# Kernel optimization log

Measured on AMD Instinct MI355X. Metric: run time of the kernel, lower is better.

The kernel has to match this reference:

```python
import jax, jax.numpy as jnp
import numpy as np

S, B, E, H, Q, T, K, N = 256, 32, 768, 1024, 64, 512, 11, 16
STD = 2.5
EPS = 1e-5


def gaussian_kernel(size, std):
    t = np.linspace(-(size - 1) / 2, (size - 1) / 2, size)
    x, y = np.meshgrid(t, t)
    kern = np.exp(-0.5 * (x ** 2 + y ** 2) / std ** 2)
    return (kern / kern.sum()).astype(np.float32)


def setup_inputs() -> dict:
    key = jax.random.key(0)
    ks = jax.random.split(key, 24)
    s = 0.05
    inp = {
        'sentence_batch': jax.random.normal(ks[0], (S, B, E), jnp.float32),
        # forward LSTM params (torch layout: W_ih (4H,E), W_hh (4H,H), gate order i,f,g,o)
        'Wih_f': jax.random.normal(ks[1], (4 * H, E), jnp.float32) * s,
        'Whh_f': jax.random.normal(ks[2], (4 * H, H), jnp.float32) * s,
        'bih_f': jnp.zeros((4 * H,), jnp.float32),
        'bhh_f': jnp.zeros((4 * H,), jnp.float32),
        # backward LSTM params
        'Wih_b': jax.random.normal(ks[3], (4 * H, E), jnp.float32) * s,
        'Whh_b': jax.random.normal(ks[4], (4 * H, H), jnp.float32) * s,
        'bih_b': jnp.zeros((4 * H,), jnp.float32),
        'bhh_b': jnp.zeros((4 * H,), jnp.float32),
        # layer norms
        'g_in': jnp.ones((E,), jnp.float32), 'be_in': jnp.zeros((E,), jnp.float32),
        'g_fw': jnp.ones((H,), jnp.float32), 'be_fw': jnp.zeros((H,), jnp.float32),
        'g_bk': jnp.ones((H,), jnp.float32), 'be_bk': jnp.zeros((H,), jnp.float32),
        'g_sq': jnp.ones((2 * Q,), jnp.float32), 'be_sq': jnp.zeros((2 * Q,), jnp.float32),
        # squeeze + topic linears (torch layout: W (out,in))
        'Wsq': jax.random.normal(ks[5], (Q, H), jnp.float32) * s,
        'bsq': jnp.zeros((Q,), jnp.float32),
        'Wtop': jax.random.normal(ks[6], (T, 2 * Q), jnp.float32) * s,
        'btop': jnp.zeros((T,), jnp.float32),
        'gauss_kern': jnp.asarray(gaussian_kernel(K, STD)),
    }
    return inp


def layer_norm(x, g, b):
    mu = jnp.mean(x, axis=-1, keepdims=True)
    var = jnp.mean((x - mu) ** 2, axis=-1, keepdims=True)
    return g * (x - mu) * jax.lax.rsqrt(var + EPS) + b


def lstm(x, Wih, Whh, bih, bhh):
    # x: (S, B, E) -> hidden states (S, B, H). torch gate order: i, f, g, o.
    h0 = jnp.zeros((x.shape[1], Whh.shape[1]), x.dtype)
    c0 = jnp.zeros_like(h0)
    xg = jnp.einsum('sbe,ge->sbg', x, Wih) + bih  # precompute input gates

    def step(carry, xt):
        h, c = carry
        gates = xt + h @ Whh.T + bhh
        i, f, g, o = jnp.split(gates, 4, axis=-1)
        c = jax.nn.sigmoid(f) * c + jax.nn.sigmoid(i) * jnp.tanh(g)
        h = jax.nn.sigmoid(o) * jnp.tanh(c)
        return (h, c), h

    _, hs = jax.lax.scan(step, (h0, c0), xg)
    return hs


def batch_pca(e, dim):
    # e: (S, B, F) -> projections (B, S, dim) onto top-dim principal axes
    c = e - jnp.mean(e, axis=0)
    cov = jnp.einsum('sbi,sbj->bij', c, c) / e.shape[0]  # (B, F, F), symmetric
    _, evecs = jnp.linalg.eigh(cov)  # ascending eigenvalues
    top = evecs[:, :, ::-1][:, :, :dim]  # (B, F, dim), descending order
    return jnp.einsum('sbf,bfn->bsn', c, top)


def gauss_smooth(x, kern):
    # x: (B, S, N) smoothed with 2D gaussian, SAME padding
    p = (kern.shape[0] - 1) // 2
    y = jax.lax.conv_general_dilated(
        x[:, None, :, :], kern[None, None, :, :], (1, 1), [(p, p), (p, p)])
    return y[:, 0]


def adj_cos(e):
    # cosine similarity between adjacent sequence positions: (B, S, N) -> (B, S-1)
    a, b = e[:, :-1], e[:, 1:]
    num = jnp.sum(a * b, axis=-1)
    den = jnp.linalg.norm(a, axis=-1) * jnp.linalg.norm(b, axis=-1)
    return num / den


def reference(sentence_batch, Wih_f, Whh_f, bih_f, bhh_f, Wih_b, Whh_b, bih_b, bhh_b,
              g_in, be_in, g_fw, be_fw, g_bk, be_bk, g_sq, be_sq,
              Wsq, bsq, Wtop, btop, gauss_kern):
    x = layer_norm(sentence_batch, g_in, be_in)
    x_f = lstm(x, Wih_f, Whh_f, bih_f, bhh_f)
    x_b = lstm(x[::-1], Wih_b, Whh_b, bih_b, bhh_b)[::-1]
    x_f = layer_norm(x_f, g_fw, be_fw)
    x_b = layer_norm(x_b, g_bk, be_bk)
    x_f = jnp.tanh(jnp.einsum('sbh,qh->sbq', x_f, Wsq) + bsq)
    x_b = jnp.tanh(jnp.einsum('sbh,qh->sbq', x_b, Wsq) + bsq)
    xc = layer_norm(jnp.concatenate((x_f, x_b), axis=-1), g_sq, be_sq)
    topic_preds = jnp.einsum('sbq,tq->sbt', xc, Wtop) + btop

    # segmentation path (no-grad in original)
    e_f = batch_pca(jax.lax.stop_gradient(x_f), N)
    e_b = batch_pca(jax.lax.stop_gradient(x_b), N)
    e_f = gauss_smooth(e_f, gauss_kern)
    e_b = gauss_smooth(e_b, gauss_kern)
    d = jnp.sqrt(adj_cos(e_f) * adj_cos(e_b))  # (B, S-1)
    pos = jnp.argmax(d, axis=1)
    return topic_preds, pos
```

## Files before the change

kernel.cpp:

```cpp
#include <hip/hip_runtime.h>
#include <cstdint>
#include <cstddef>

#define SS   256
#define BB   32
#define EE   768
#define HH   1024
#define QQ   64
#define TTOP 512
#define NPC  16
#define G4   4096
#define TCHUNK 32
#define NBLK 256
#define EPSF 1e-5f

#define OFF_XNT   ((size_t)0)
#define OFF_WHHT  ((size_t)6291456)
#define OFF_CT    ((size_t)14680064)
#define OFF_HBUF  ((size_t)14745600)
#define OFF_CNT   ((size_t)14876672)
#define OFF_XG    ((size_t)14877184)
#define OFF_HS    ((size_t)23265792)
#define OFF_XQ    ((size_t)40043008)
#define OFF_CMAT  ((size_t)0)
#define OFF_COV   ((size_t)1048576)
#define OFF_PG    ((size_t)1310720)
#define OFF_COS   ((size_t)1376256)

#define WLKS 4616
#define LSTM_DYN_LDS 161536

#define AST 65
#define EIG_DYN_LDS 133120

#define EPS32D    5.9604644775390625e-8
#define EPS232D   (EPS32D*EPS32D)
#define SAFMIN32D 1.1754943508222875e-38

__device__ __forceinline__ float sigm(float x){ return 1.0f/(1.0f + expf(-x)); }

__device__ __forceinline__ double wsumd(double v){
  #pragma unroll
  for (int o = 32; o; o >>= 1) v += __shfl_xor(v, o, 64);
  return v;
}
__device__ __forceinline__ double wmaxd(double v){
  #pragma unroll
  for (int o = 32; o; o >>= 1) v = fmax(v, __shfl_xor(v, o, 64));
  return v;
}
__device__ __forceinline__ void dlartg_(double f, double g, double& c, double& s, double& r){
  if (g == 0.0){ c = 1.0; s = 0.0; r = f; }
  else if (f == 0.0){ c = 0.0; s = (g >= 0.0) ? 1.0 : -1.0; r = fabs(g); }
  else {
    double d = sqrt(f*f + g*g);
    c = fabs(f)/d;
    r = copysign(d, f);
    s = g/r;
  }
}
__device__ void dlaev2_(double a, double b, double c,
                        double& rt1, double& rt2, double& cs1, double& sn1){
  double sm = a + c, df = a - c, adf = fabs(df), tb = b + b, ab = fabs(tb);
  double acmx, acmn;
  if (fabs(a) > fabs(c)){ acmx = a; acmn = c; } else { acmx = c; acmn = a; }
  double rt;
  if (adf > ab)      rt = adf*sqrt(1.0 + (ab/adf)*(ab/adf));
  else if (adf < ab) rt = ab*sqrt(1.0 + (adf/ab)*(adf/ab));
  else               rt = ab*sqrt(2.0);
  int sgn1;
  if (sm < 0.0){ rt1 = 0.5*(sm - rt); sgn1 = -1; rt2 = (acmx/rt1)*acmn - (b/rt1)*b; }
  else if (sm > 0.0){ rt1 = 0.5*(sm + rt); sgn1 = 1; rt2 = (acmx/rt1)*acmn - (b/rt1)*b; }
  else { rt1 = 0.5*rt; rt2 = -0.5*rt; sgn1 = 1; }
  double cs; int sgn2;
  if (df >= 0.0){ cs = df + rt; sgn2 = 1; } else { cs = df - rt; sgn2 = -1; }
  double acs = fabs(cs);
  if (acs > ab){ double ct = -tb/cs; sn1 = 1.0/sqrt(1.0+ct*ct); cs1 = ct*sn1; }
  else {
    if (ab == 0.0){ cs1 = 1.0; sn1 = 0.0; }
    else { double tn = -cs/tb; cs1 = 1.0/sqrt(1.0+tn*tn); sn1 = tn*cs1; }
  }
  if (sgn1 == sgn2){ double tn = cs1; cs1 = -sn1; sn1 = tn; }
}

__device__ void dsteqr16_(int base, double* d, double* e, double* z16, int ln){
  if (ln < 16){
    #pragma unroll
    for (int j = 0; j < 16; j++) z16[ln*17+j] = (ln==j) ? 1.0 : 0.0;
  }
  const int n = 16, nm1 = 15;
  int jtot = 0; const int nmaxit = 480;
  int l1 = 0;
  while (l1 < n){
    if (l1 > 0) e[base+l1-1] = 0.0;
    int m = nm1;
    for (int mm = l1; mm < nm1; mm++){
      double tst = fabs(e[base+mm]);
      if (tst == 0.0){ m = mm; break; }
      if (tst <= (sqrt(fabs(d[base+mm]))*sqrt(fabs(d[base+mm+1])))*EPS32D){
        e[base+mm] = 0.0; m = mm; break;
      }
    }
    int l = l1, lend = m;
    l1 = m + 1;
    if (lend == l) continue;
    if (fabs(d[base+lend]) < fabs(d[base+l])){ int t = l; l = lend; lend = t; }
    if (lend > l){
      for (;;){
        int mm = lend;
        for (int k2 = l; k2 < lend; k2++){
          double tst = e[base+k2]*e[base+k2];
          if (tst <= (EPS232D*fabs(d[base+k2]))*fabs(d[base+k2+1]) + SAFMIN32D){ mm = k2; break; }
        }
        if (mm < lend) e[base+mm] = 0.0;
        double p = d[base+l];
        if (mm == l){ l++; if (l <= lend) continue; break; }
        if (mm == l+1){
          double rt1, rt2, cc, ss;
          dlaev2_(d[base+l], e[base+l], d[base+l+1], rt1, rt2, cc, ss);
          if (ln < 16){
            double x = z16[ln*17+l], y = z16[ln*17+l+1];
            z16[ln*17+l]   = cc*x + ss*y;
            z16[ln*17+l+1] = cc*y - ss*x;
          }
          d[base+l] = rt1; d[base+l+1] = rt2; e[base+l] = 0.0;
          l += 2; if (l <= lend) continue; break;
        }
        if (jtot == nmaxit) break;
        jtot++;
        double g = (d[base+l+1]-p)/(2.0*e[base+l]);
        double r = sqrt(g*g+1.0);
        g = d[base+mm] - p + e[base+l]/(g + copysign(r, g));
        double s2 = 1.0, c2 = 1.0; p = 0.0;
        for (int i = mm-1; i >= l; i--){
          double f = s2*e[base+i], b = c2*e[base+i];
          dlartg_(g, f, c2, s2, r);
          if (i != mm-1) e[base+i+1] = r;
          g = d[base+i+1] - p;
          r = (d[base+i]-g)*s2 + 2.0*c2*b;
          p = s2*r;
          d[base+i+1] = g + p;
          g = c2*r - b;
          if (ln < 16){
            double x = z16[ln*17+i], y = z16[ln*17+i+1];
            z16[ln*17+i]   = c2*x - s2*y;
            z16[ln*17+i+1] = s2*x + c2*y;
          }
        }
        d[base+l] -= p; e[base+l] = g;
      }
    } else {
      for (;;){
        int mm = lend;
        for (int k2 = l; k2 > lend; k2--){
          double tst = e[base+k2-1]*e[base+k2-1];
          if (tst <= (EPS232D*fabs(d[base+k2]))*fabs(d[base+k2-1]) + SAFMIN32D){ mm = k2; break; }
        }
        if (mm > lend) e[base+mm-1] = 0.0;
        double p = d[base+l];
        if (mm == l){ l--; if (l >= lend) continue; break; }
        if (mm == l-1){
          double rt1, rt2, cc, ss;
          dlaev2_(d[base+l-1], e[base+l-1], d[base+l], rt1, rt2, cc, ss);
          if (ln < 16){
            double x = z16[ln*17+l-1], y = z16[ln*17+l];
            z16[ln*17+l-1] = cc*x + ss*y;
            z16[ln*17+l]   = cc*y - ss*x;
          }
          d[base+l-1] = rt1; d[base+l] = rt2; e[base+l-1] = 0.0;
          l -= 2; if (l >= lend) continue; break;
        }
        if (jtot == nmaxit) break;
        jtot++;
        double g = (d[base+l-1]-p)/(2.0*e[base+l-1]);
        double r = sqrt(g*g+1.0);
        g = d[base+mm] - p + e[base+l-1]/(g + copysign(r, g));
        double s2 = 1.0, c2 = 1.0; p = 0.0;
        for (int i = mm; i <= l-1; i++){
          double f = s2*e[base+i], b = c2*e[base+i];
          dlartg_(g, f, c2, s2, r);
          if (i != mm) e[base+i-1] = r;
          g = d[base+i] - p;
          r = (d[base+i+1]-g)*s2 + 2.0*c2*b;
          p = s2*r;
          d[base+i] = g + p;
          g = c2*r - b;
          if (ln < 16){
            double x = z16[ln*17+i], y = z16[ln*17+i+1];
            z16[ln*17+i]   = c2*x + s2*y;
            z16[ln*17+i+1] = c2*y - s2*x;
          }
        }
        d[base+l] -= p; e[base+l-1] = g;
      }
    }
  }
  for (int ii = 1; ii < n; ii++){
    int i = ii-1, k = i; double p = d[base+i];
    for (int j = ii; j < n; j++) if (d[base+j] < p){ k = j; p = d[base+j]; }
    if (k != i){
      d[base+k] = d[base+i]; d[base+i] = p;
      if (ln < 16){ double t = z16[ln*17+i]; z16[ln*17+i] = z16[ln*17+k]; z16[ln*17+k] = t; }
    }
  }
}

__device__ void dc_merge(int base, int n1, int n2, double rho_in, int tid,
    double* s_d, double* Zt, double* Tt,
    double* md, double* mz, double* dl, double* wz, double* lam, double* zh,
    double* ev, double* su4, int* indx, int* sec, int* defl, int* prm,
    int* sKn){
  const int ln = tid & 63, w = tid >> 6;
  int n = n1 + n2;
  double zv = 0.0;
  if (ln < n){
    if (ln < n1) zv = Zt[(size_t)(base+n1-1)*AST + base + ln];
    else         zv = Zt[(size_t)(base+n1)*AST + base + ln];
    if (rho_in < 0.0 && ln >= n1) zv = -zv;
  }
  zv *= 0.70710678118654752440;
  mz[ln] = (ln < n) ? zv : 0.0;
  md[ln] = (ln < n) ? s_d[base+ln] : 0.0;
  __syncthreads();
  double rho = fabs(2.0*rho_in);
  if (tid == 0){
    int i1 = 0, i2 = n1, k = 0;
    while (i1 < n1 && i2 < n){
      if (md[i2] < md[i1]) indx[k++] = i2++; else indx[k++] = i1++;
    }
    while (i1 < n1) indx[k++] = i1++;
    while (i2 < n)  indx[k++] = i2++;
  }
  __syncthreads();
  double dmax = wmaxd((ln<n) ? fabs(md[ln]) : 0.0);
  double zmax = wmaxd((ln<n) ? fabs(mz[ln]) : 0.0);
  double tol = 8.0*EPS32D*fmax(dmax, zmax);
  if (w == 0){
    int K = 0, ndefl = 0, pj = -1;
    for (int j = 0; j < n; j++){
      int nj = indx[j];
      if (rho*fabs(mz[nj]) <= tol){
        defl[ndefl++] = nj;
      } else if (pj < 0){
        pj = nj;
      } else {
        double sG = mz[pj], cG = mz[nj];
        double tau = sqrt(cG*cG + sG*sG);
        double tdf = md[nj] - md[pj];
        double c = cG/tau, s = -sG/tau;
        if (fabs(tdf*c*s) <= tol){
          mz[nj] = tau; mz[pj] = 0.0;
          if (ln < n){
            double x = Zt[(size_t)(base+ln)*AST + base+pj];
            double y = Zt[(size_t)(base+ln)*AST + base+nj];
            Zt[(size_t)(base+ln)*AST + base+pj] = c*x + s*y;
            Zt[(size_t)(base+ln)*AST + base+nj] = c*y - s*x;
          }
          double t2 = md[pj]*c*c + md[nj]*s*s;
          double t3 = md[pj]*s*s + md[nj]*c*c;
          md[nj] = t3; md[pj] = t2;
          defl[ndefl++] = pj;
          pj = nj;
        } else {
          sec[K] = pj; dl[K] = md[pj]; wz[K] = mz[pj]; K++;
          pj = nj;
        }
      }
    }
    if (pj >= 0){ sec[K] = pj; dl[K] = md[pj]; wz[K] = mz[pj]; K++; }
    if (ln == 0){ sKn[0] = K; sKn[1] = ndefl; }
  }
  __syncthreads();
  const int K = sKn[0], ndefl = sKn[1];
  double wsum2 = wsumd((ln < K) ? wz[ln]*wz[ln] : 0.0);
  if (ln < K){
    double lo = dl[ln];
    double hi = (ln < K-1) ? dl[ln+1] : (dl[K-1] + rho*wsum2);
    for (int it = 0; it < 120; it++){
      double mid = 0.5*(lo+hi);
      if (!(mid > lo) || !(mid < hi)) break;
      double fv = 1.0;
      for (int i2 = 0; i2 < K; i2++) fv += rho*wz[i2]*wz[i2]/(dl[i2]-mid);
      if (fv < 0.0) lo = mid; else hi = mid;
    }
    double lj = 0.5*(lo+hi);
    if (!(lj > dl[ln])) lj = nextafter(dl[ln], 1.0e300);
    lam[ln] = lj;
  }
  __syncthreads();
  if (ln < K){
    double di = dl[ln];
    double prod = lam[K-1] - di;
    for (int j2 = 0; j2 < ln; j2++)   prod *= (lam[j2]-di)/(dl[j2]-di);
    for (int j2 = ln; j2 < K-1; j2++) prod *= (lam[j2]-di)/(dl[j2+1]-di);
    zh[ln] = copysign(sqrt(fabs(prod)), wz[ln]);
  }
  __syncthreads();
  for (int j = w; j < K; j += 4){
    double ui = (ln < K) ? zh[ln]/(dl[ln]-lam[j]) : 0.0;
    double nrm = sqrt(wsumd(ui*ui));
    su4[w*64 + ln] = ui/nrm;
    if (ln < n){
      double acc = 0.0;
      for (int i2 = 0; i2 < K; i2++)
        acc += Zt[(size_t)(base+ln)*AST + base + sec[i2]]*su4[w*64 + i2];
      Tt[(size_t)ln*AST + j] = acc;
    }
    if (ln == 0) ev[j] = lam[j];
  }
  __syncthreads();
  for (int j = 0; j < ndefl; j++){
    int cj = defl[j];
    if (ln < n) Tt[(size_t)ln*AST + K + j] = Zt[(size_t)(base+ln)*AST + base + cj];
    if (ln == 0) ev[K+j] = md[cj];
  }
  __syncthreads();
  if (tid == 0){
    for (int i2 = 0; i2 < n; i2++) prm[i2] = i2;
    for (int a2 = 0; a2 < n-1; a2++){
      int kk = a2;
      for (int b2 = a2+1; b2 < n; b2++) if (ev[prm[b2]] < ev[prm[kk]]) kk = b2;
      int t3 = prm[a2]; prm[a2] = prm[kk]; prm[kk] = t3;
    }
  }
  __syncthreads();
  if (ln < n){
    for (int c2 = 0; c2 < n; c2++)
      Zt[(size_t)(base+ln)*AST + base + c2] = Tt[(size_t)ln*AST + prm[c2]];
  }
  if (ln == 0){ for (int c2 = 0; c2 < n; c2++) s_d[base+c2] = ev[prm[c2]]; }
  __syncthreads();
}

__global__ __launch_bounds__(256) void k_eig(const float* __restrict__ covg,
                                             float* __restrict__ Pg){
  int u = blockIdx.x, tid = threadIdx.x;
  const int ln = tid & 63, w = tid >> 6;
  extern __shared__ double dsm[];
  double* A  = dsm;
  double* Qh = dsm + 4160;
  double* Zt = dsm + 8320;
  double* Tt = dsm + 12480;
  __shared__ double s_d[64], s_e[64], s_tau[64], s_v[64], s_w[64];
  __shared__ double md[64], mz[64], dl[64], wz[64], lam[64], zh[64], ev[64];
  __shared__ double su4[4*64];
  __shared__ double z16a[4*272];
  __shared__ int indx[64], sec[64], defl[64], prm[64], sKn[2];

  for (int n = tid; n < 4096; n += 256)
    A[(n >> 6)*AST + (n & 63)] = (double)covg[(size_t)u*4096 + n];
  __syncthreads();

  for (int i = 0; i < 63; i++){
    double alpha = A[(size_t)(i+1)*AST + i];
    double xv = (ln >= i+2) ? A[(size_t)ln*AST + i] : 0.0;
    double xnorm2 = wsumd(xv*xv);
    if (xnorm2 == 0.0){
      if (tid == 0){ s_e[i] = alpha; s_tau[i] = 0.0; }
    } else {
      double beta = -copysign(sqrt(alpha*alpha + xnorm2), alpha);
      double taui = (beta - alpha)/beta;
      double sc = 1.0/(alpha - beta);
      s_v[ln] = (ln == i+1) ? 1.0 : ((ln >= i+2) ? A[(size_t)ln*AST+i]*sc : 0.0);
      __syncthreads();
      if (ln >= i+2) A[(size_t)ln*AST+i] = s_v[ln];
      double wr = 0.0;
      if (ln >= i+1){
        for (int c2 = i+1; c2 < 64; c2++){
          double av = (ln >= c2) ? A[(size_t)ln*AST+c2] : A[(size_t)c2*AST+ln];
          wr += av*s_v[c2];
        }
        wr *= taui;
      }
      double dotwv = wsumd((ln >= i+1) ? wr*s_v[ln] : 0.0);
      double alp2 = -0.5*taui*dotwv;
      wr += alp2*s_v[ln];
      s_w[ln] = (ln >= i+1) ? wr : 0.0;
      __syncthreads();
      if (ln >= i+1){
        for (int c2 = i+1; c2 <= ln; c2++)
          if ((c2 & 3) == w)
            A[(size_t)ln*AST+c2] -= s_v[ln]*s_w[c2] + s_w[ln]*s_v[c2];
      }
      if (tid == 0){ s_e[i] = beta; s_tau[i] = taui; }
    }
    __syncthreads();
  }
  if (w == 0) s_d[ln] = A[(size_t)ln*AST+ln];
  __syncthreads();

  for (int n = tid; n < 4160; n += 256) Qh[n] = 0.0;
  __syncthreads();
  if (w == 0) Qh[(size_t)ln*AST+ln] = 1.0;
  __syncthreads();
  for (int i = 62; i >= 0; i--){
    double taui = s_tau[i];
    if (taui != 0.0){
      s_v[ln] = (ln == i+1) ? 1.0 : ((ln >= i+2) ? A[(size_t)ln*AST+i] : 0.0);
      __syncthreads();
      double dj = 0.0;
      for (int r2 = i+1; r2 < 64; r2++) dj += s_v[r2]*Qh[(size_t)r2*AST+ln];
      dj *= taui;
      for (int r2 = i+1; r2 < 64; r2++)
        if ((r2 & 3) == w)
          Qh[(size_t)r2*AST+ln] -= s_v[r2]*dj;
    }
    __syncthreads();
  }

  double rho_a = s_e[15], rho_b = s_e[47], rho_top = s_e[31];
  if (tid == 0){
    s_d[15] -= fabs(rho_a);   s_d[16] -= fabs(rho_a);
    s_d[31] -= fabs(rho_top); s_d[32] -= fabs(rho_top);
    s_d[47] -= fabs(rho_b);   s_d[48] -= fabs(rho_b);
  }
  for (int n = tid; n < 4160; n += 256) Zt[n] = 0.0;
  __syncthreads();
  dsteqr16_(w*16, s_d, s_e, &z16a[w*272], ln);
  if (ln < 16){
    for (int j = 0; j < 16; j++)
      Zt[(size_t)(w*16+ln)*AST + w*16 + j] = z16a[w*272 + ln*17+j];
  }
  __syncthreads();

  dc_merge(0, 16, 16, rho_a, tid, s_d, Zt, Tt, md, mz, dl, wz, lam, zh, ev, su4, indx, sec, defl, prm, sKn);
  dc_merge(32, 16, 16, rho_b, tid, s_d, Zt, Tt, md, mz, dl, wz, lam, zh, ev, su4, indx, sec, defl, prm, sKn);
  dc_merge(0, 32, 32, rho_top, tid, s_d, Zt, Tt, md, mz, dl, wz, lam, zh, ev, su4, indx, sec, defl, prm, sKn);

  for (int nn = w; nn < 16; nn += 4){
    double acc = 0.0;
    for (int k = 0; k < 64; k++)
      acc += Qh[(size_t)ln*AST+k]*Zt[(size_t)k*AST + (63-nn)];
    Pg[(size_t)u*1024 + ln*16 + nn] = (float)acc;
  }
}

__global__ void k_ln_in(const float* __restrict__ x, const float* __restrict__ g,
                        const float* __restrict__ be, float* __restrict__ xnT){
  int bid = blockIdx.x; int s = bid >> 5, b = bid & 31;
  int tid = threadIdx.x;
  const float* row = x + ((size_t)(s*BB + b))*EE;
  __shared__ float r1[256], r2[256];
  float su = 0.f, sq = 0.f;
  for (int e = tid; e < EE; e += 256){ float v = row[e]; su += v; sq += v*v; }
  r1[tid] = su; r2[tid] = sq; __syncthreads();
  for (int st = 128; st > 0; st >>= 1){
    if (tid < st){ r1[tid] += r1[tid+st]; r2[tid] += r2[tid+st]; }
    __syncthreads();
  }
  float mu  = r1[0] * (1.0f/EE);
  float var = r2[0] * (1.0f/EE) - mu*mu;
  float rstd = rsqrtf(var + EPSF);
  for (int e = tid; e < EE; e += 256){
    float v = (row[e]-mu)*rstd*g[e] + be[e];
    xnT[((size_t)s*EE + e)*BB + b] = v;
  }
}

__global__ void k_whht(const float* __restrict__ Whh_f, const float* __restrict__ Whh_b,
                       float* __restrict__ WhhT){
  int d  = blockIdx.z;
  const float* Whh = d ? Whh_b : Whh_f;
  int rt = blockIdx.x*32, kt = blockIdx.y*32;
  int tx = threadIdx.x & 31, ty = threadIdx.x >> 5;
  __shared__ float tile[32][33];
  for (int i = ty; i < 32; i += 8)
    tile[i][tx] = Whh[(size_t)(rt+i)*HH + kt+tx];
  __syncthreads();
  for (int i = ty; i < 32; i += 8)
    WhhT[((size_t)d*HH + kt+i)*G4 + rt+tx] = tile[tx][i];
}

__global__ void k_zero(float* __restrict__ p, int n){
  int i = blockIdx.x*blockDim.x + threadIdx.x;
  if (i < n) p[i] = 0.f;
}

__global__ __launch_bounds__(256) void k_xg(const float* __restrict__ xnT,
        const float* __restrict__ Wih_f, const float* __restrict__ Wih_b,
        float* __restrict__ xg, int* __restrict__ cnt, int c){
  if (blockIdx.x == 0 && blockIdx.y == 0 && threadIdx.x < 17)
    __hip_atomic_store(&cnt[threadIdx.x*16], 0, __ATOMIC_RELAXED, __HIP_MEMORY_SCOPE_AGENT);
  int nb = blockIdx.x, rb = blockIdx.y;
  int d = rb >> 5, rloc0 = (rb & 31)*128;
  const float* Wih = d ? Wih_b : Wih_f;
  int tid = threadIdx.x;
  int tx = tid & 15, ty = tid >> 4;
  __shared__ float Al[16*132];
  __shared__ float Bl[16*132];
  float acc[8][8];
  #pragma unroll
  for (int i = 0; i < 8; i++)
    #pragma unroll
    for (int j = 0; j < 8; j++) acc[i][j] = 0.f;
  for (int kc = 0; kc < EE; kc += 16){
    #pragma unroll
    for (int j = 0; j < 8; j++){
      int idx = tid + j*256;
      int n = idx & 127, k = idx >> 7;
      int tglob = c*TCHUNK + nb*4 + (n >> 5);
      int tsrc = d ? (SS-1-tglob) : tglob;
      Al[k*132 + n] = xnT[((size_t)tsrc*EE + kc + k)*BB + (n & 31)];
    }
    #pragma unroll
    for (int j = 0; j < 8; j++){
      int idx = tid + j*256;
      int k = idx & 15, r = idx >> 4;
      Bl[k*132 + r] = Wih[(size_t)(rloc0 + r)*EE + kc + k];
    }
    __syncthreads();
    #pragma unroll
    for (int k = 0; k < 16; k++){
      float4 a0 = *(const float4*)(&Al[k*132 + tx*4]);
      float4 a1 = *(const float4*)(&Al[k*132 + 64 + tx*4]);
      float4 b0 = *(const float4*)(&Bl[k*132 + ty*4]);
      float4 b1 = *(const float4*)(&Bl[k*132 + 64 + ty*4]);
      float av[8] = {a0.x,a0.y,a0.z,a0.w,a1.x,a1.y,a1.z,a1.w};
      float bv[8] = {b0.x,b0.y,b0.z,b0.w,b1.x,b1.y,b1.z,b1.w};
      #pragma unroll
      for (int i = 0; i < 8; i++)
        #pragma unroll
        for (int j2 = 0; j2 < 8; j2++) acc[i][j2] += av[i]*bv[j2];
    }
    __syncthreads();
  }
  #pragma unroll
  for (int j = 0; j < 8; j++){
    int r = rloc0 + ((j < 4) ? (ty*4 + j) : (64 + ty*4 + j - 4));
    #pragma unroll
    for (int ig = 0; ig < 2; ig++){
      int n0 = ig*64 + tx*4;
      int tl = nb*4 + (n0 >> 5), b = n0 & 31;
      float4 o = make_float4(acc[ig*4+0][j], acc[ig*4+1][j], acc[ig*4+2][j], acc[ig*4+3][j]);
      *(float4*)(&xg[(((size_t)tl*8192) + d*G4 + r)*BB + b]) = o;
    }
  }
}

__global__ __launch_bounds__(256) void k_lstm(
    const float* __restrict__ WhhT,
    const float* __restrict__ bih_f, const float* __restrict__ bhh_f,
    const float* __restrict__ bih_b, const float* __restrict__ bhh_b,
    const float* __restrict__ xg, float* __restrict__ hbuf,
    float* __restrict__ cT, float* __restrict__ hs,
    int* __restrict__ cnt, int c)
{
  extern __shared__ float lsm[];
  float* Wl  = lsm;
  float* red = lsm + 36928;
  float* gl  = lsm + 38976;
  float* cls = lsm + 40128;

  const int blk = blockIdx.x;
  const int d   = blk >> 7;
  const int j0  = (blk & 127) * 8;
  const int tid = threadIdx.x;
  const int ln  = tid & 63;
  const int w   = tid >> 6;
  const int cg  = ln >> 3;
  const int bg  = ln & 7;
  const int b0  = bg * 4;
  const int cbase = cg * 4;

  const float* bih = d ? bih_b : bih_f;
  const float* bhh = d ? bhh_b : bhh_f;
  const float* WT_d = WhhT + (size_t)d * HH * G4;

  {
    const int cs = tid & 31;
    const int ks = tid >> 5;
    const int g  = cs >> 3, jj = cs & 7;
    const size_t rglob = (size_t)g*HH + j0 + jj;
    for (int kk = 0; kk < 128; kk++){
      int k = kk*8 + ks;
      Wl[(k >> 7)*WLKS + (k & 127)*36 + cs] = WT_d[(size_t)k*G4 + rglob];
    }
  }

  const int pjj = tid >> 5, pb = tid & 31;
  cls[pjj*32 + pb] = cT[((size_t)d*HH + j0 + pjj)*BB + pb];
  float pbias[4];
  #pragma unroll
  for (int g2 = 0; g2 < 4; g2++)
    pbias[g2] = bih[g2*HH + j0 + pjj] + bhh[g2*HH + j0 + pjj];
  __syncthreads();

  for (int tl = 0; tl < TCHUNK; tl++){
    const int s = c*TCHUNK + tl;
    const float* hprev = hbuf + ((size_t)((s & 1)*2 + d))*HH*BB;
    float*       hnext = hbuf + ((size_t)(((s+1) & 1)*2 + d))*HH*BB;

    float xgv[4];
    {
      const size_t xbase = ((size_t)tl*8192 + (size_t)d*G4)*BB;
      #pragma unroll
      for (int g2 = 0; g2 < 4; g2++)
        xgv[g2] = xg[xbase + (size_t)(g2*HH + j0 + pjj)*BB + pb];
    }

    float acc[4][4];
    #pragma unroll
    for (int i = 0; i < 4; i++)
      #pragma unroll
      for (int j = 0; j < 4; j++) acc[i][j] = 0.f;

    {
      const float* hp = hprev + (size_t)(w*256)*BB + b0;
      for (int ib = 0; ib < 256; ib += 16){
        float4 hv[16];
        #pragma unroll
        for (int u = 0; u < 16; u++)
          hv[u] = *(const float4*)(hp + (size_t)(ib+u)*BB);
        #pragma unroll
        for (int u = 0; u < 16; u++){
          int k = w*256 + ib + u;
          float4 wv = *(const float4*)(&Wl[(k >> 7)*WLKS + (k & 127)*36 + cbase]);
          acc[0][0] += wv.x*hv[u].x; acc[0][1] += wv.x*hv[u].y; acc[0][2] += wv.x*hv[u].z; acc[0][3] += wv.x*hv[u].w;
          acc[1][0] += wv.y*hv[u].x; acc[1][1] += wv.y*hv[u].y; acc[1][2] += wv.y*hv[u].z; acc[1][3] += wv.y*hv[u].w;
          acc[2][0] += wv.z*hv[u].x; acc[2][1] += wv.z*hv[u].y; acc[2][2] += wv.z*hv[u].z; acc[2][3] += wv.z*hv[u].w;
          acc[3][0] += wv.w*hv[u].x; acc[3][1] += wv.w*hv[u].y; acc[3][2] += wv.w*hv[u].z; acc[3][3] += wv.w*hv[u].w;
        }
      }
    }
    if (w == 1 || w == 3){
      float* rp = &red[(w >> 1)*1024 + ln*16];
      #pragma unroll
      for (int i = 0; i < 4; i++)
        #pragma unroll
        for (int j = 0; j < 4; j++) rp[i*4+j] = acc[i][j];
    }
    __syncthreads();
    if (w == 0 || w == 2){
      const float* rp = &red[(w >> 1)*1024 + ln*16];
      #pragma unroll
      for (int i = 0; i < 4; i++)
        #pragma unroll
        for (int j = 0; j < 4; j++) acc[i][j] += rp[i*4+j];
    }
    __syncthreads();
    if (w == 2){
      float* rp = &red[ln*16];
      #pragma unroll
      for (int i = 0; i < 4; i++)
        #pragma unroll
        for (int j = 0; j < 4; j++) rp[i*4+j] = acc[i][j];
    }
    __syncthreads();
    if (w == 0){
      const float* rp = &red[ln*16];
      #pragma unroll
      for (int i = 0; i < 4; i++){
        #pragma unroll
        for (int j = 0; j < 4; j++) acc[i][j] += rp[i*4+j];
        float4 o = make_float4(acc[i][0], acc[i][1], acc[i][2], acc[i][3]);
        *(float4*)(&gl[(cbase + i)*36 + b0]) = o;
      }
    }
    __syncthreads();
    {
      float gv[4];
      #pragma unroll
      for (int g2 = 0; g2 < 4; g2++)
        gv[g2] = gl[(g2*8 + pjj)*36 + pb] + pbias[g2] + xgv[g2];
      float iv = sigm(gv[0]), fv = sigm(gv[1]), ggv = tanhf(gv[2]), ov = sigm(gv[3]);
      float cv = fv*cls[pjj*32 + pb] + iv*ggv;
      cls[pjj*32 + pb] = cv;
      float h = ov*tanhf(cv);
      hnext[(size_t)(j0 + pjj)*BB + pb] = h;
      int tsv = d ? (SS-1-s) : s;
      hs[(((size_t)d*SS + tsv)*HH + j0 + pjj)*BB + pb] = h;
    }
    if (tl < TCHUNK-1){
      __syncthreads();
      if (tid == 0){
        __builtin_amdgcn_fence(__ATOMIC_RELEASE, "agent");
        __hip_atomic_fetch_add(&cnt[(blk & 15)*16], 1, __ATOMIC_RELAXED, __HIP_MEMORY_SCOPE_AGENT);
        const int target = 16*(tl+1);
        if (blk == 0){
          int done = 0;
          while (done < 16){
            done = 0;
            #pragma unroll
            for (int i = 0; i < 16; i++)
              done += (__hip_atomic_load(&cnt[i*16], __ATOMIC_RELAXED, __HIP_MEMORY_SCOPE_AGENT) >= target);
            if (done < 16) __builtin_amdgcn_s_sleep(2);
          }
          __hip_atomic_store(&cnt[256], tl+1, __ATOMIC_RELAXED, __HIP_MEMORY_SCOPE_AGENT);
        } else {
          while (__hip_atomic_load(&cnt[256], __ATOMIC_RELAXED, __HIP_MEMORY_SCOPE_AGENT) < tl+1)
            __builtin_amdgcn_s_sleep(2);
        }
        __builtin_amdgcn_fence(__ATOMIC_ACQUIRE, "agent");
      }
      __syncthreads();
    }
  }
  __syncthreads();
  cT[((size_t)d*HH + j0 + pjj)*BB + pb] = cls[pjj*32 + pb];
}

__global__ __launch_bounds__(256) void k_lnproj(const float* __restrict__ hs,
        const float* __restrict__ g_fw, const float* __restrict__ be_fw,
        const float* __restrict__ g_bk, const float* __restrict__ be_bk,
        const float* __restrict__ Wsq, const float* __restrict__ bsq,
        float* __restrict__ xq){
  int t = blockIdx.x, d = blockIdx.y;
  int tid = threadIdx.x;
  const float* gv  = d ? g_bk  : g_fw;
  const float* bev = d ? be_bk : be_fw;
  const float* hrow = hs + ((size_t)d*SS + t)*HH*BB;
  __shared__ float red[256], red2[256];
  __shared__ float smu[32], srs[32];
  __shared__ float ln[32*132];
  __shared__ float wl[64*132];
  {
    int b = tid & 31, jg = tid >> 5;
    float s = 0.f, s2 = 0.f;
    for (int j = jg*128; j < jg*128+128; j++){
      float v = hrow[(size_t)j*BB + b];
      s += v; s2 += v*v;
    }
    red[b*8 + jg] = s; red2[b*8 + jg] = s2; __syncthreads();
    if (tid < 32){
      float a = 0.f, a2 = 0.f;
      for (int k = 0; k < 8; k++){ a += red[tid*8+k]; a2 += red2[tid*8+k]; }
      float mu = a*(1.f/HH), var = a2*(1.f/HH) - mu*mu;
      smu[tid] = mu; srs[tid] = rsqrtf(var + EPSF);
    }
    __syncthreads();
  }
  float acc[4][2] = {{0.f,0.f},{0.f,0.f},{0.f,0.f},{0.f,0.f}};
  int qg = tid & 31, bg = tid >> 5;
  int q0 = qg*2, b0g = bg*4;
  for (int jc = 0; jc < 8; jc++){
    for (int n = tid; n < 4096; n += 256){
      int b = n & 31, jj = n >> 5; int j = jc*128 + jj;
      float v = hrow[(size_t)j*BB + b];
      ln[b*132+jj] = (v - smu[b])*srs[b]*gv[j] + bev[j];
    }
    for (int n = tid; n < 8192; n += 256){
      int q = n >> 7, jj = n & 127;
      wl[q*132+jj] = Wsq[(size_t)q*HH + jc*128 + jj];
    }
    __syncthreads();
    for (int jj = 0; jj < 128; jj += 4){
      float4 w0 = *(const float4*)(&wl[q0*132+jj]);
      float4 w1 = *(const float4*)(&wl[(q0+1)*132+jj]);
      #pragma unroll
      for (int i = 0; i < 4; i++){
        float4 xv = *(const float4*)(&ln[(b0g+i)*132+jj]);
        acc[i][0] += xv.x*w0.x + xv.y*w0.y + xv.z*w0.z + xv.w*w0.w;
        acc[i][1] += xv.x*w1.x + xv.y*w1.y + xv.z*w1.z + xv.w*w1.w;
      }
    }
    __syncthreads();
  }
  #pragma unroll
  for (int i = 0; i < 4; i++)
    #pragma unroll
    for (int u = 0; u < 2; u++){
      float o = tanhf(acc[i][u] + bsq[q0+u]);
      xq[(((size_t)d*SS + t)*BB + (b0g+i))*QQ + q0 + u] = o;
    }
}

__global__ __launch_bounds__(256) void k_topic(const float* __restrict__ xq,
        const float* __restrict__ g_sq, const float* __restrict__ be_sq,
        const float* __restrict__ Wtop, const float* __restrict__ btop,
        float* __restrict__ out){
  int t = blockIdx.x; int tid = threadIdx.x;
  __shared__ float xc[32*132];
  __shared__ float wl[16*520];
  __shared__ float red[256], red2[256];
  __shared__ float smu[32], srs[32];
  for (int n = tid; n < 4096; n += 256){
    int b = n >> 7, q = n & 127;
    float v = (q < 64) ? xq[(((size_t)0*SS + t)*BB + b)*QQ + q]
                       : xq[(((size_t)1*SS + t)*BB + b)*QQ + (q-64)];
    xc[b*132+q] = v;
  }
  __syncthreads();
  {
    int b = tid >> 3, sl = tid & 7;
    float s = 0.f, s2 = 0.f;
    for (int k = 0; k < 16; k++){ float v = xc[b*132 + sl*16 + k]; s += v; s2 += v*v; }
    red[tid] = s; red2[tid] = s2; __syncthreads();
    if (tid < 32){
      float a = 0.f, a2 = 0.f;
      for (int k = 0; k < 8; k++){ a += red[tid*8+k]; a2 += red2[tid*8+k]; }
      float mu = a*(1.f/128.f), var = a2*(1.f/128.f) - mu*mu;
      smu[tid] = mu; srs[tid] = rsqrtf(var + EPSF);
    }
    __syncthreads();
    for (int n = tid; n < 4096; n += 256){
      int b2 = n >> 7, q = n & 127;
      xc[b2*132+q] = (xc[b2*132+q]-smu[b2])*srs[b2]*g_sq[q] + be_sq[q];
    }
    __syncthreads();
  }
  int og = tid & 63, bg = tid >> 6;
  int o0 = og*8, b0 = bg*8;
  float acc[8][8];
  #pragma unroll
  for (int i = 0; i < 8; i++)
    #pragma unroll
    for (int j = 0; j < 8; j++) acc[i][j] = 0.f;
  for (int kc = 0; kc < 128; kc += 16){
    for (int n = tid; n < 8192; n += 256){
      int o = n >> 4, kk = n & 15;
      wl[kk*520 + o] = Wtop[(size_t)o*128 + kc + kk];
    }
    __syncthreads();
    #pragma unroll
    for (int kk = 0; kk < 16; kk++){
      float4 w0 = *(const float4*)(&wl[kk*520+o0]);
      float4 w1 = *(const float4*)(&wl[kk*520+o0+4]);
      float wv[8] = {w0.x,w0.y,w0.z,w0.w,w1.x,w1.y,w1.z,w1.w};
      int k = kc + kk;
      #pragma unroll
      for (int bi = 0; bi < 8; bi++){
        float xv = xc[(b0+bi)*132 + k];
        #pragma unroll
        for (int oi = 0; oi < 8; oi++) acc[bi][oi] += xv*wv[oi];
      }
    }
    __syncthreads();
  }
  #pragma unroll
  for (int bi = 0; bi < 8; bi++){
    int b = b0 + bi;
    #pragma unroll
    for (int oi = 0; oi < 8; oi++)
      out[((size_t)t*BB + b)*TTOP + o0 + oi] = acc[bi][oi] + btop[o0+oi];
  }
}

__global__ __launch_bounds__(256) void k_pca1(const float* __restrict__ xq,
        float* __restrict__ cmat, float* __restrict__ covg){
  int u = blockIdx.x; int d = u >> 5, b = u & 31;
  int tid = threadIdx.x;
  __shared__ float red[256];
  __shared__ float smq[64];
  {
    int q = tid & 63, tg = tid >> 6;
    float s = 0.f;
    for (int t2 = tg*64; t2 < tg*64+64; t2++)
      s += xq[(((size_t)d*SS + t2)*BB + b)*QQ + q];
    red[tid] = s; __syncthreads();
    if (tid < 64) smq[tid] = (red[tid]+red[tid+64]+red[tid+128]+red[tid+192])*(1.f/SS);
    __syncthreads();
  }
  float* cm = cmat + (size_t)u*SS*QQ;
  for (int n = tid; n < SS*QQ; n += 256){
    int t2 = n >> 6, q = n & 63;
    cm[n] = xq[(((size_t)d*SS + t2)*BB + b)*QQ + q] - smq[q];
  }
  __syncthreads();
  {
    int pg = (tid & 15)*4, qg = (tid >> 4)*4;
    float a[4][4] = {{0}};
    for (int t2 = 0; t2 < SS; t2++){
      const float* cr = cm + (size_t)t2*QQ;
      float4 cp = *(const float4*)(cr+pg);
      float4 cq = *(const float4*)(cr+qg);
      float pv[4] = {cp.x,cp.y,cp.z,cp.w}, qv[4] = {cq.x,cq.y,cq.z,cq.w};
      #pragma unroll
      for (int i = 0; i < 4; i++)
        #pragma unroll
        for (int j2 = 0; j2 < 4; j2++) a[i][j2] += pv[i]*qv[j2];
    }
    #pragma unroll
    for (int i = 0; i < 4; i++)
      #pragma unroll
      for (int j2 = 0; j2 < 4; j2++)
        covg[(size_t)u*4096 + (pg+i)*64 + qg+j2] = a[i][j2]*(1.f/SS);
  }
}

__global__ __launch_bounds__(256) void k_pca2(const float* __restrict__ cmat,
        const float* __restrict__ Pg, const float* __restrict__ kern,
        float* __restrict__ cosb){
  int u = blockIdx.x; int tid = threadIdx.x;
  __shared__ float sP[1024];
  __shared__ float sE[4096];
  __shared__ float sY[4096];
  __shared__ float kb[121];
  __shared__ float nn2[256];
  if (tid < 121) kb[tid] = kern[tid];
  for (int n = tid; n < 1024; n += 256) sP[n] = Pg[(size_t)u*1024 + n];
  __syncthreads();
  const float* cm = cmat + (size_t)u*SS*QQ;
  for (int m = tid; m < SS*NPC; m += 256){
    int t2 = m >> 4, n = m & 15;
    const float* cr = cm + (size_t)t2*QQ;
    float acc = 0.f;
    for (int i = 0; i < 64; i++) acc += cr[i]*sP[i*16+n];
    sE[m] = acc;
  }
  __syncthreads();
  for (int m = tid; m < SS*NPC; m += 256){
    int t2 = m >> 4, n = m & 15;
    float acc = 0.f;
    for (int a2 = 0; a2 < 11; a2++){
      int ta = t2 + a2 - 5;
      if (ta < 0 || ta >= SS) continue;
      #pragma unroll
      for (int b2 = 0; b2 < 11; b2++){
        int nb = n + b2 - 5;
        if (nb < 0 || nb >= NPC) continue;
        acc += kb[a2*11+b2]*sE[ta*16+nb];
      }
    }
    sY[m] = acc;
  }
  __syncthreads();
  {
    float acc = 0.f;
    #pragma unroll
    for (int n = 0; n < 16; n++){ float v = sY[tid*16+n]; acc += v*v; }
    nn2[tid] = acc;
  }
  __syncthreads();
  if (tid < 255){
    float num = 0.f;
    #pragma unroll
    for (int n = 0; n < 16; n++) num += sY[tid*16+n]*sY[(tid+1)*16+n];
    cosb[(size_t)u*256 + tid] = num/(sqrtf(nn2[tid])*sqrtf(nn2[tid+1]));
  }
}

__global__ void k_pos(const float* __restrict__ cosb, float* __restrict__ out){
  __shared__ float mx[256];
  __shared__ int   mi[256];
  int tid = threadIdx.x;
  for (int b = 0; b < 32; b++){
    float v = -1e30f;
    if (tid < 255){
      float cf = cosb[(size_t)(b)*256 + tid];
      float cb = cosb[(size_t)(32+b)*256 + tid];
      v = sqrtf(cf*cb);
      if (isnan(v)) v = INFINITY;
    }
    mx[tid] = v; __syncthreads();
    for (int st = 128; st > 0; st >>= 1){
      if (tid < st) mx[tid] = fmaxf(mx[tid], mx[tid+st]);
      __syncthreads();
    }
    float m = mx[0]; __syncthreads();
    mi[tid] = (tid < 255 && v == m) ? tid : (1<<30);
    __syncthreads();
    for (int st = 128; st > 0; st >>= 1){
      if (tid < st) mi[tid] = min(mi[tid], mi[tid+st]);
      __syncthreads();
    }
    if (tid == 0) out[(size_t)SS*BB*TTOP + b] = (float)mi[0];
    __syncthreads();
  }
}

extern "C" void kernel_launch(void* const* d_in, const int* in_sizes, int n_in,
                              void* d_out, int out_size, void* d_ws, size_t ws_size,
                              hipStream_t stream){
  (void)in_sizes; (void)n_in; (void)out_size; (void)ws_size;
  const float* x      = (const float*)d_in[0];
  const float* Wih_f  = (const float*)d_in[1];
  const float* Whh_f  = (const float*)d_in[2];
  const float* bih_f  = (const float*)d_in[3];
  const float* bhh_f  = (const float*)d_in[4];
  const float* Wih_b  = (const float*)d_in[5];
  const float* Whh_b  = (const float*)d_in[6];
  const float* bih_b  = (const float*)d_in[7];
  const float* bhh_b  = (const float*)d_in[8];
  const float* g_in   = (const float*)d_in[9];
  const float* be_in  = (const float*)d_in[10];
  const float* g_fw   = (const float*)d_in[11];
  const float* be_fw  = (const float*)d_in[12];
  const float* g_bk   = (const float*)d_in[13];
  const float* be_bk  = (const float*)d_in[14];
  const float* g_sq   = (const float*)d_in[15];
  const float* be_sq  = (const float*)d_in[16];
  const float* Wsq    = (const float*)d_in[17];
  const float* bsq    = (const float*)d_in[18];
  const float* Wtop   = (const float*)d_in[19];
  const float* btop   = (const float*)d_in[20];
  const float* gkern  = (const float*)d_in[21];

  float* ws    = (float*)d_ws;
  float* xnT   = ws + OFF_XNT;
  float* WhhT  = ws + OFF_WHHT;
  float* cT    = ws + OFF_CT;
  float* hbuf  = ws + OFF_HBUF;
  int*   cnt   = (int*)(ws + OFF_CNT);
  float* xg    = ws + OFF_XG;
  float* hs    = ws + OFF_HS;
  float* xq    = ws + OFF_XQ;
  float* cmat  = ws + OFF_CMAT;
  float* covg  = ws + OFF_COV;
  float* Pg    = ws + OFF_PG;
  float* cosb  = ws + OFF_COS;
  float* out   = (float*)d_out;

  hipFuncSetAttribute((const void*)k_eig,
                      hipFuncAttributeMaxDynamicSharedMemorySize, EIG_DYN_LDS);
  hipFuncSetAttribute((const void*)k_lstm,
                      hipFuncAttributeMaxDynamicSharedMemorySize, LSTM_DYN_LDS);

  k_zero<<<dim3(768), dim3(256), 0, stream>>>(cT, 196608);
  k_ln_in<<<dim3(SS*BB), dim3(256), 0, stream>>>(x, g_in, be_in, xnT);
  k_whht<<<dim3(128, 32, 2), dim3(256), 0, stream>>>(Whh_f, Whh_b, WhhT);
  for (int c = 0; c < SS/TCHUNK; c++){
    k_xg<<<dim3(8, 64), dim3(256), 0, stream>>>(xnT, Wih_f, Wih_b, xg, cnt, c);
    k_lstm<<<dim3(NBLK), dim3(256), LSTM_DYN_LDS, stream>>>(WhhT, bih_f, bhh_f, bih_b, bhh_b,
                                                            xg, hbuf, cT, hs, cnt, c);
  }
  k_lnproj<<<dim3(SS,2), dim3(256), 0, stream>>>(hs, g_fw, be_fw, g_bk, be_bk, Wsq, bsq, xq);
  k_topic<<<dim3(SS), dim3(256), 0, stream>>>(xq, g_sq, be_sq, Wtop, btop, out);
  k_pca1<<<dim3(64), dim3(256), 0, stream>>>(xq, cmat, covg);
  k_eig<<<dim3(64), dim3(256), EIG_DYN_LDS, stream>>>(covg, Pg);
  k_pca2<<<dim3(64), dim3(256), 0, stream>>>(cmat, Pg, gkern, cosb);
  k_pos<<<dim3(1), dim3(256), 0, stream>>>(cosb, out);
}
```

Measured before the change: 9.021 ms.

## Widen LSTM blocks, shuffle-reduce gates, split grid barrier per direction, parallelize secular bisection

The recurrent LSTM kernel now runs 512 threads per block. The K dimension is split across eight lanes groups within each wavefront, and partial gate sums are combined with cross-lane shuffles, replacing the shared-memory reduction and its extra barriers. The grid-wide step barrier is split into independent forward and backward counters and flags, so each direction only waits on its own 128 blocks. In the eigen solver, the secular-equation bisection now spreads the sum over terms across four waves, using a block-wide count to stop early, trading extra syncthreads per iteration for shorter serial loops.

Measured after the change: 7.489 ms. 1.2x faster.

```diff
diff --git a/kernel.cpp b/kernel.cpp
--- a/kernel.cpp
+++ b/kernel.cpp
@@ -28,7 +28,7 @@
 #define OFF_COS   ((size_t)1376256)
 
 #define WLKS 4616
-#define LSTM_DYN_LDS 161536
+#define LSTM_DYN_LDS 153344
 
 #define AST 65
 #define EIG_DYN_LDS 133120
@@ -273,19 +273,40 @@
   __syncthreads();
   const int K = sKn[0], ndefl = sKn[1];
   double wsum2 = wsumd((ln < K) ? wz[ln]*wz[ln] : 0.0);
-  if (ln < K){
-    double lo = dl[ln];
-    double hi = (ln < K-1) ? dl[ln+1] : (dl[K-1] + rho*wsum2);
+  {
+    bool conv = (ln >= K);
+    double lo = 0.0, hi = 0.0;
+    if (!conv){
+      lo = dl[ln];
+      hi = (ln < K-1) ? dl[ln+1] : (dl[K-1] + rho*wsum2);
+    }
+    const int i2lo = w*16;
     for (int it = 0; it < 120; it++){
-      double mid = 0.5*(lo+hi);
-      if (!(mid > lo) || !(mid < hi)) break;
-      double fv = 1.0;
-      for (int i2 = 0; i2 < K; i2++) fv += rho*wz[i2]*wz[i2]/(dl[i2]-mid);
-      if (fv < 0.0) lo = mid; else hi = mid;
-    }
-    double lj = 0.5*(lo+hi);
-    if (!(lj > dl[ln])) lj = nextafter(dl[ln], 1.0e300);
-    lam[ln] = lj;
+      double mid = 0.0;
+      if (!conv){
+        mid = 0.5*(lo+hi);
+        if (!(mid > lo) || !(mid < hi)) conv = true;
+      }
+      double fp = 0.0;
+      if (!conv){
+        int i2hi = i2lo + 16; if (i2hi > K) i2hi = K;
+        for (int i2 = i2lo; i2 < i2hi; i2++)
+          fp += rho*wz[i2]*wz[i2]/(dl[i2]-mid);
+      }
+      su4[w*64 + ln] = fp;
+      int alldone = __syncthreads_count(conv ? 1 : 0);
+      if (alldone == 256) break;
+      if (!conv){
+        double fv = 1.0 + su4[ln] + su4[64+ln] + su4[128+ln] + su4[192+ln];
+        if (fv < 0.0) lo = mid; else hi = mid;
+      }
+      __syncthreads();
+    }
+    if (ln < K){
+      double lj = 0.5*(lo+hi);
+      if (!(lj > dl[ln])) lj = nextafter(dl[ln], 1.0e300);
+      lam[ln] = lj;
+    }
   }
   __syncthreads();
   if (ln < K){
@@ -479,8 +500,12 @@
 __global__ __launch_bounds__(256) void k_xg(const float* __restrict__ xnT,
         const float* __restrict__ Wih_f, const float* __restrict__ Wih_b,
         float* __restrict__ xg, int* __restrict__ cnt, int c){
-  if (blockIdx.x == 0 && blockIdx.y == 0 && threadIdx.x < 17)
-    __hip_atomic_store(&cnt[threadIdx.x*16], 0, __ATOMIC_RELAXED, __HIP_MEMORY_SCOPE_AGENT);
+  if (blockIdx.x == 0 && blockIdx.y == 0){
+    if (threadIdx.x < 17)
+      __hip_atomic_store(&cnt[threadIdx.x*16], 0, __ATOMIC_RELAXED, __HIP_MEMORY_SCOPE_AGENT);
+    else if (threadIdx.x == 17)
+      __hip_atomic_store(&cnt[384], 0, __ATOMIC_RELAXED, __HIP_MEMORY_SCOPE_AGENT);
+  }
   int nb = blockIdx.x, rb = blockIdx.y;
   int d = rb >> 5, rloc0 = (rb & 31)*128;
   const float* Wih = d ? Wih_b : Wih_f;
@@ -537,7 +562,7 @@
   }
 }
 
-__global__ __launch_bounds__(256) void k_lstm(
+__global__ __launch_bounds__(512) void k_lstm(
     const float* __restrict__ WhhT,
     const float* __restrict__ bih_f, const float* __restrict__ bhh_f,
     const float* __restrict__ bih_b, const float* __restrict__ bhh_b,
@@ -547,9 +572,8 @@
 {
   extern __shared__ float lsm[];
   float* Wl  = lsm;
-  float* red = lsm + 36928;
-  float* gl  = lsm + 38976;
-  float* cls = lsm + 40128;
+  float* gl  = lsm + 36928;
+  float* cls = lsm + 38080;
 
   const int blk = blockIdx.x;
   const int d   = blk >> 7;
@@ -557,10 +581,10 @@
   const int tid = threadIdx.x;
   const int ln  = tid & 63;
   const int w   = tid >> 6;
-  const int cg  = ln >> 3;
-  const int bg  = ln & 7;
-  const int b0  = bg * 4;
-  const int cbase = cg * 4;
+  const int ksub = ln >> 3;
+  const int bg   = ln & 7;
+  const int b0   = bg * 4;
+  const int cbase = w * 4;
 
   const float* bih = d ? bih_b : bih_f;
   const float* bhh = d ? bhh_b : bhh_f;
@@ -571,18 +595,20 @@
     const int ks = tid >> 5;
     const int g  = cs >> 3, jj = cs & 7;
     const size_t rglob = (size_t)g*HH + j0 + jj;
-    for (int kk = 0; kk < 128; kk++){
-      int k = kk*8 + ks;
+    for (int kk = 0; kk < 64; kk++){
+      int k = kk*16 + ks;
       Wl[(k >> 7)*WLKS + (k & 127)*36 + cs] = WT_d[(size_t)k*G4 + rglob];
     }
   }
 
-  const int pjj = tid >> 5, pb = tid & 31;
-  cls[pjj*32 + pb] = cT[((size_t)d*HH + j0 + pjj)*BB + pb];
+  const int pjj = (tid >> 5) & 7, pb = tid & 31;
   float pbias[4];
-  #pragma unroll
-  for (int g2 = 0; g2 < 4; g2++)
-    pbias[g2] = bih[g2*HH + j0 + pjj] + bhh[g2*HH + j0 + pjj];
+  if (tid < 256){
+    cls[pjj*32 + pb] = cT[((size_t)d*HH + j0 + pjj)*BB + pb];
+    #pragma unroll
+    for (int g2 = 0; g2 < 4; g2++)
+      pbias[g2] = bih[g2*HH + j0 + pjj] + bhh[g2*HH + j0 + pjj];
+  }
   __syncthreads();
 
   for (int tl = 0; tl < TCHUNK; tl++){
@@ -590,8 +616,8 @@
     const float* hprev = hbuf + ((size_t)((s & 1)*2 + d))*HH*BB;
     float*       hnext = hbuf + ((size_t)(((s+1) & 1)*2 + d))*HH*BB;
 
-    float xgv[4];
-    {
+    float xgv[4] = {0.f,0.f,0.f,0.f};
+    if (tid < 256){
       const size_t xbase = ((size_t)tl*8192 + (size_t)d*G4)*BB;
       #pragma unroll
       for (int g2 = 0; g2 < 4; g2++)
@@ -605,16 +631,16 @@
       for (int j = 0; j < 4; j++) acc[i][j] = 0.f;
 
     {
-      const float* hp = hprev + (size_t)(w*256)*BB + b0;
-      for (int ib = 0; ib < 256; ib += 16){
+      const float* hp = hprev + (size_t)(ksub*128)*BB + b0;
+      const float* wrow = &Wl[ksub*WLKS + cbase];
+      for (int ib = 0; ib < 128; ib += 16){
         float4 hv[16];
         #pragma unroll
         for (int u = 0; u < 16; u++)
           hv[u] = *(const float4*)(hp + (size_t)(ib+u)*BB);
         #pragma unroll
         for (int u = 0; u < 16; u++){
-          int k = w*256 + ib + u;
-          float4 wv = *(const float4*)(&Wl[(k >> 7)*WLKS + (k & 127)*36 + cbase]);
+          float4 wv = *(const float4*)(wrow + (ib+u)*36);
           acc[0][0] += wv.x*hv[u].x; acc[0][1] += wv.x*hv[u].y; acc[0][2] += wv.x*hv[u].z; acc[0][3] += wv.x*hv[u].w;
           acc[1][0] += wv.y*hv[u].x; acc[1][1] += wv.y*hv[u].y; acc[1][2] += wv.y*hv[u].z; acc[1][3] += wv.y*hv[u].w;
           acc[2][0] += wv.z*hv[u].x; acc[2][1] += wv.z*hv[u].y; acc[2][2] += wv.z*hv[u].z; acc[2][3] += wv.z*hv[u].w;
@@ -622,42 +648,25 @@
         }
       }
     }
-    if (w == 1 || w == 3){
-      float* rp = &red[(w >> 1)*1024 + ln*16];
+    #pragma unroll
+    for (int i = 0; i < 4; i++)
       #pragma unroll
-      for (int i = 0; i < 4; i++)
-        #pragma unroll
-        for (int j = 0; j < 4; j++) rp[i*4+j] = acc[i][j];
-    }
-    __syncthreads();
-    if (w == 0 || w == 2){
-      const float* rp = &red[(w >> 1)*1024 + ln*16];
-      #pragma unroll
-      for (int i = 0; i < 4; i++)
-        #pragma unroll
-        for (int j = 0; j < 4; j++) acc[i][j] += rp[i*4+j];
-    }
-    __syncthreads();
-    if (w == 2){
-      float* rp = &red[ln*16];
-      #pragma unroll
-      for (int i = 0; i < 4; i++)
-        #pragma unroll
-        for (int j = 0; j < 4; j++) rp[i*4+j] = acc[i][j];
-    }
-    __syncthreads();
-    if (w == 0){
-      const float* rp = &red[ln*16];
+      for (int j = 0; j < 4; j++){
+        float v = acc[i][j];
+        v += __shfl_xor(v, 8, 64);
+        v += __shfl_xor(v, 16, 64);
+        v += __shfl_xor(v, 32, 64);
+        acc[i][j] = v;
+      }
+    if (ksub == 0){
       #pragma unroll
       for (int i = 0; i < 4; i++){
-        #pragma unroll
-        for (int j = 0; j < 4; j++) acc[i][j] += rp[i*4+j];
         float4 o = make_float4(acc[i][0], acc[i][1], acc[i][2], acc[i][3]);
         *(float4*)(&gl[(cbase + i)*36 + b0]) = o;
       }
     }
     __syncthreads();
-    {
+    if (tid < 256){
       float gv[4];
       #pragma unroll
       for (int g2 = 0; g2 < 4; g2++)
@@ -674,20 +683,22 @@
       __syncthreads();
       if (tid == 0){
         __builtin_amdgcn_fence(__ATOMIC_RELEASE, "agent");
-        __hip_atomic_fetch_add(&cnt[(blk & 15)*16], 1, __ATOMIC_RELAXED, __HIP_MEMORY_SCOPE_AGENT);
+        __hip_atomic_fetch_add(&cnt[((blk & 7) + d*8)*16], 1, __ATOMIC_RELAXED, __HIP_MEMORY_SCOPE_AGENT);
         const int target = 16*(tl+1);
-        if (blk == 0){
+        const int flagidx = d ? 384 : 256;
+        if ((blk & 127) == 0){
+          const int lbase = d*8;
           int done = 0;
-          while (done < 16){
+          while (done < 8){
             done = 0;
             #pragma unroll
-            for (int i = 0; i < 16; i++)
-              done += (__hip_atomic_load(&cnt[i*16], __ATOMIC_RELAXED, __HIP_MEMORY_SCOPE_AGENT) >= target);
-            if (done < 16) __builtin_amdgcn_s_sleep(2);
+            for (int i = 0; i < 8; i++)
+              done += (__hip_atomic_load(&cnt[(lbase+i)*16], __ATOMIC_RELAXED, __HIP_MEMORY_SCOPE_AGENT) >= target);
+            if (done < 8) __builtin_amdgcn_s_sleep(2);
           }
-          __hip_atomic_store(&cnt[256], tl+1, __ATOMIC_RELAXED, __HIP_MEMORY_SCOPE_AGENT);
+          __hip_atomic_store(&cnt[flagidx], tl+1, __ATOMIC_RELAXED, __HIP_MEMORY_SCOPE_AGENT);
         } else {
-          while (__hip_atomic_load(&cnt[256], __ATOMIC_RELAXED, __HIP_MEMORY_SCOPE_AGENT) < tl+1)
+          while (__hip_atomic_load(&cnt[flagidx], __ATOMIC_RELAXED, __HIP_MEMORY_SCOPE_AGENT) < tl+1)
             __builtin_amdgcn_s_sleep(2);
         }
         __builtin_amdgcn_fence(__ATOMIC_ACQUIRE, "agent");
@@ -696,7 +707,8 @@
     }
   }
   __syncthreads();
-  cT[((size_t)d*HH + j0 + pjj)*BB + pb] = cls[pjj*32 + pb];
+  if (tid < 256)
+    cT[((size_t)d*HH + j0 + pjj)*BB + pb] = cls[pjj*32 + pb];
 }
 
 __global__ __launch_bounds__(256) void k_lnproj(const float* __restrict__ hs,
@@ -1010,7 +1022,7 @@
   k_whht<<<dim3(128, 32, 2), dim3(256), 0, stream>>>(Whh_f, Whh_b, WhhT);
   for (int c = 0; c < SS/TCHUNK; c++){
     k_xg<<<dim3(8, 64), dim3(256), 0, stream>>>(xnT, Wih_f, Wih_b, xg, cnt, c);
-    k_lstm<<<dim3(NBLK), dim3(256), LSTM_DYN_LDS, stream>>>(WhhT, bih_f, bhh_f, bih_b, bhh_b,
+    k_lstm<<<dim3(NBLK), dim3(512), LSTM_DYN_LDS, stream>>>(WhhT, bih_f, bhh_f, bih_b, bhh_b,
                                                             xg, hbuf, cT, hs, cnt, c);
   }
   k_lnproj<<<dim3(SS,2), dim3(256), 0, stream>>>(hs, g_fw, be_fw, g_bk, be_bk, Wsq, bsq, xq);
```
